# Performance work log

Measured on AMD Instinct MI355X. Metric: run time of the kernel, lower is better.

The kernel has to match this reference:

```python
import jax, jax.numpy as jnp
import numpy as np

D_MODEL = 1024
NUM_HEADS = 16
HEAD_DIM = D_MODEL // NUM_HEADS
B, S = 4, 2048


def setup_inputs() -> dict:
    key = jax.random.key(0)
    ks = jax.random.split(key, 11)
    scale = 1.0 / np.sqrt(D_MODEL)
    inp = {
        "query": jax.random.normal(ks[0], (B, S, D_MODEL), dtype=jnp.float32),
        "key": jax.random.normal(ks[1], (B, S, D_MODEL), dtype=jnp.float32),
        "value": jax.random.normal(ks[2], (B, S, D_MODEL), dtype=jnp.float32),
        "Wq": jax.random.normal(ks[3], (D_MODEL, D_MODEL), dtype=jnp.float32) * scale,
        "bq": jnp.zeros((D_MODEL,), dtype=jnp.float32),
        "Wk": jax.random.normal(ks[4], (D_MODEL, D_MODEL), dtype=jnp.float32) * scale,
        "bk": jnp.zeros((D_MODEL,), dtype=jnp.float32),
        "Wv": jax.random.normal(ks[5], (D_MODEL, D_MODEL), dtype=jnp.float32) * scale,
        "bv": jnp.zeros((D_MODEL,), dtype=jnp.float32),
        "Wo": jax.random.normal(ks[6], (D_MODEL, D_MODEL), dtype=jnp.float32) * scale,
        "bo": jnpp.zeros((D_MODEL,), dtype=jnp.float32) if False else jnp.zeros((D_MODEL,), dtype=jnp.float32),
    }
    return inp


def reference(query, key, value, Wq, bq, Wk, bk, Wv, bv, Wo, bo):
    # Linear projections (torch Linear: x @ W.T + b), split into heads: [B,H,S,Dh]
    def split_heads(x):
        b, s, _ = x.shape
        return x.reshape(b, s, NUM_HEADS, HEAD_DIM).transpose(0, 2, 1, 3)

    q = split_heads(query @ Wq.T + bq)
    k = split_heads(key @ Wk.T + bk)
    v = split_heads(value @ Wv.T + bv)

    # Explicit attention: [B,H,S,S] scores, softmax, AV
    scores = jnp.einsum("bhqd,bhkd->bhqk", q, k) / np.sqrt(HEAD_DIM).astype(np.float32)
    attn = jax.nn.softmax(scores, axis=-1)
    ctx = jnp.einsum("bhqk,bhkd->bhqd", attn, v)

    # Merge heads and output projection
    b = ctx.shape[0]
    ctx = ctx.transpose(0, 2, 1, 3).reshape(b, -1, D_MODEL)
    return ctx @ Wo.T + bo
```

## Files before the change

kernel.cpp:

```cpp
#include <hip/hip_runtime.h>
#include <stdint.h>

#define DMODEL 1024
#define NHEADS 16
#define HDIM   64
#define BB     4
#define SS     2048
#define MM     (BB*SS)
#define QKV_ELEMS ((size_t)8388608)

typedef unsigned short ushort_t;
typedef __bf16    bf16x8  __attribute__((ext_vector_type(8)));
typedef _Float16  half4   __attribute__((ext_vector_type(4)));
typedef _Float16  half2_t __attribute__((ext_vector_type(2)));
typedef float     floatx4 __attribute__((ext_vector_type(4)));

__device__ inline ushort_t f32_to_bf16(float f) {
    union { float f; uint32_t u; } v; v.f = f;
    uint32_t r = v.u + 0x7FFF + ((v.u >> 16) & 1);
    return (ushort_t)(r >> 16);
}
__device__ inline ushort_t f32_to_f16u(float f) {
    union { _Float16 h; ushort_t u; } v; v.h = (_Float16)f; return v.u;
}
__device__ inline half2_t pkrtz(float a, float b) {
    return __builtin_bit_cast(half2_t, __builtin_amdgcn_cvt_pkrtz(a, b));
}
__device__ inline void glds16(const void* g, void* l) {
    __builtin_amdgcn_global_load_lds(
        (const __attribute__((address_space(1))) unsigned int*)g,
        (__attribute__((address_space(3))) unsigned int*)l, 16, 0, 0);
}

__global__ __launch_bounds__(256) void convert_bf16(const float* __restrict__ in,
                                                    ushort_t* __restrict__ out) {
    size_t i = ((size_t)blockIdx.x * 256 + threadIdx.x) * 8;
    float4 a = *(const float4*)&in[i];
    float4 b = *(const float4*)&in[i + 4];
    ushort_t t[8];
    t[0] = f32_to_bf16(a.x); t[1] = f32_to_bf16(a.y);
    t[2] = f32_to_bf16(a.z); t[3] = f32_to_bf16(a.w);
    t[4] = f32_to_bf16(b.x); t[5] = f32_to_bf16(b.y);
    t[6] = f32_to_bf16(b.z); t[7] = f32_to_bf16(b.w);
    *(uint4*)&out[i] = *(uint4*)t;
}

__global__ __launch_bounds__(256) void convert_w3(
    const float* __restrict__ w0, const float* __restrict__ w1, const float* __restrict__ w2,
    ushort_t* __restrict__ o0, ushort_t* __restrict__ o1, ushort_t* __restrict__ o2) {
    const float* src = (blockIdx.y == 0) ? w0 : (blockIdx.y == 1) ? w1 : w2;
    ushort_t*    dst = (blockIdx.y == 0) ? o0 : (blockIdx.y == 1) ? o1 : o2;
    size_t i = ((size_t)blockIdx.x * 256 + threadIdx.x) * 8;
    float4 a = *(const float4*)&src[i];
    float4 b = *(const float4*)&src[i + 4];
    ushort_t t[8];
    t[0] = f32_to_bf16(a.x); t[1] = f32_to_bf16(a.y);
    t[2] = f32_to_bf16(a.z); t[3] = f32_to_bf16(a.w);
    t[4] = f32_to_bf16(b.x); t[5] = f32_to_bf16(b.y);
    t[6] = f32_to_bf16(b.z); t[7] = f32_to_bf16(b.w);
    *(uint4*)&dst[i] = *(uint4*)t;
}

template<int OUT>
__global__ __launch_bounds__(256) void gemm_bf16(
    const ushort_t* __restrict__ A, const ushort_t* __restrict__ W,
    const float* __restrict__ bias, void* __restrict__ O, float scale)
{
    __shared__ ushort_t As[2 * 128 * 32];
    __shared__ ushort_t Bs[2 * 128 * 32];

    const int tid  = threadIdx.x;
    const int lane = tid & 63;
    const int quad = lane >> 4;
    const int l15  = lane & 15;
    const int wid  = tid >> 6;
    const int wr   = wid >> 1, wc = wid & 1;
    const int m0   = blockIdx.y * 128;
    const int n0   = blockIdx.x * 128;

    floatx4 acc[4][4];
    #pragma unroll
    for (int i = 0; i < 4; i++)
        #pragma unroll
        for (int j = 0; j < 4; j++)
            acc[i][j] = (floatx4){0.f, 0.f, 0.f, 0.f};

    #pragma unroll
    for (int j = 0; j < 2; j++) {
        const int p = tid + j * 256, row = p >> 2, cc = p & 3;
        glds16(&A[(size_t)(m0 + row) * DMODEL + cc * 8], &As[p * 8]);
        glds16(&W[(size_t)(n0 + row) * DMODEL + cc * 8], &Bs[p * 8]);
    }

    for (int k0 = 0; k0 < DMODEL; k0 += 32) {
        const int cb = ((k0 >> 5) & 1) * (128 * 32);
        const int nbo = (128 * 32) - cb;
        __syncthreads();
        const int kn = (k0 + 32) & (DMODEL - 1);
        #pragma unroll
        for (int j = 0; j < 2; j++) {
            const int p = tid + j * 256, row = p >> 2, cc = p & 3;
            glds16(&A[(size_t)(m0 + row) * DMODEL + kn + cc * 8], &As[nbo + p * 8]);
            glds16(&W[(size_t)(n0 + row) * DMODEL + kn + cc * 8], &Bs[nbo + p * 8]);
        }
        bf16x8 af[4], bf[4];
        #pragma unroll
        for (int i = 0; i < 4; i++)
            af[i] = *(const bf16x8*)&As[cb + (wr * 64 + i * 16 + l15) * 32 + quad * 8];
        #pragma unroll
        for (int j = 0; j < 4; j++)
            bf[j] = *(const bf16x8*)&Bs[cb + (wc * 64 + j * 16 + l15) * 32 + quad * 8];
        #pragma unroll
        for (int i = 0; i < 4; i++)
            #pragma unroll
            for (int j = 0; j < 4; j++)
                acc[i][j] = __builtin_amdgcn_mfma_f32_16x16x32_bf16(af[i], bf[j], acc[i][j], 0, 0, 0);
    }

    #pragma unroll
    for (int j = 0; j < 4; j++) {
        const int n = n0 + wc * 64 + j * 16 + l15;
        const float bn = bias[n];
        #pragma unroll
        for (int i = 0; i < 4; i++) {
            #pragma unroll
            for (int r = 0; r < 4; r++) {
                const int m = m0 + wr * 64 + i * 16 + quad * 4 + r;
                float v = (acc[i][j][r] + bn) * scale;
                if (OUT == 0) {
                    const int b = m >> 11, s = m & 2047;
                    const int hh = n >> 6, dh = n & 63;
                    ((ushort_t*)O)[(((size_t)(b * NHEADS + hh)) * SS + s) * HDIM + dh] = f32_to_bf16(v);
                } else if (OUT == 1) {
                    const int b = m >> 11, s = m & 2047;
                    const int hh = n >> 6, dh = n & 63;
                    ((ushort_t*)O)[(((size_t)(b * NHEADS + hh)) * SS + s) * HDIM + dh] = f32_to_f16u(v);
                } else {
                    ((float*)O)[(size_t)m * DMODEL + n] = v;
                }
            }
        }
    }
}

__global__ __launch_bounds__(256, 4) void attn_kernel(
    const ushort_t* __restrict__ Q, const ushort_t* __restrict__ K,
    const ushort_t* __restrict__ V, ushort_t* __restrict__ ctx)
{
    constexpr int LDV = 72;
    constexpr int VOFF = 2 * 4096;
    __shared__ ushort_t smem[2 * 4096 + 2 * 64 * LDV];
    ushort_t* Tr = smem;

    const int tid  = threadIdx.x;
    const int lane = tid & 63;
    const int wid  = tid >> 6;
    const int quad = lane >> 4;
    const int l15  = lane & 15;
    const int bid  = blockIdx.x;
    const int bh   = (bid & 7) * 8 + (bid >> 7);
    const int b    = bh >> 4, h = bh & 15;
    const int q0   = ((bid >> 3) & 15) * 128 + wid * 32;

    const ushort_t* Qb = Q + (size_t)bh * SS * HDIM;
    const ushort_t* Kb = K + (size_t)bh * SS * HDIM;
    const ushort_t* Vb = V + (size_t)bh * SS * HDIM;

    bf16x8 qf[2][2];
    #pragma unroll
    for (int qt = 0; qt < 2; qt++)
        #pragma unroll
        for (int c = 0; c < 2; c++)
            qf[qt][c] = *(const bf16x8*)&Qb[(size_t)(q0 + qt * 16 + l15) * HDIM + c * 32 + quad * 8];

    floatx4 acc[2][4];
    #pragma unroll
    for (int qt = 0; qt < 2; qt++)
        #pragma unroll
        for (int dt = 0; dt < 4; dt++)
            acc[qt][dt] = (floatx4){0.f, 0.f, 0.f, 0.f};
    float mrun[2] = {-1e30f, -1e30f};
    float lrun[2] = {0.f, 0.f};

    const int kp = tid & 31;
    const int dc = tid >> 5;

    #pragma unroll
    for (int j = 0; j < 2; j++) {
        const int p = tid + j * 256, row = p >> 3, cc = (p & 7) ^ (row & 7);
        glds16(&Kb[(size_t)row * HDIM + cc * 8], &smem[p * 8]);
    }
    {
        ushort_t ua[8], ub[8];
        *(uint4*)ua = *(const uint4*)&Vb[(size_t)(2 * kp) * HDIM + dc * 8];
        *(uint4*)ub = *(const uint4*)&Vb[(size_t)(2 * kp + 1) * HDIM + dc * 8];
        #pragma unroll
        for (int i = 0; i < 8; i++)
            *(uint32_t*)&smem[VOFF + (dc * 8 + i) * LDV + 2 * kp] = (uint32_t)ua[i] | ((uint32_t)ub[i] << 16);
    }

    const half2_t one2 = {(_Float16)1.f, (_Float16)1.f};

    for (int kt = 0; kt < SS; kt += 64) {
        const int cur = ((kt >> 6) & 1);
        const int ko  = cur * 4096;
        const int kon = 4096 - ko;
        const int vo  = VOFF + cur * (64 * LDV);
        const int von = VOFF + (64 * LDV) - cur * (64 * LDV);
        __syncthreads();

        const int ktn = (kt + 64) & (SS - 1);
        #pragma unroll
        for (int j = 0; j < 2; j++) {
            const int p = tid + j * 256, row = p >> 3, cc = (p & 7) ^ (row & 7);
            glds16(&Kb[(size_t)(ktn + row) * HDIM + cc * 8], &smem[kon + p * 8]);
        }
        ushort_t ua[8], ub[8];
        *(uint4*)ua = *(const uint4*)&Vb[(size_t)(ktn + 2 * kp) * HDIM + dc * 8];
        *(uint4*)ub = *(const uint4*)&Vb[(size_t)(ktn + 2 * kp + 1) * HDIM + dc * 8];

        bf16x8 kf[4][2];
        #pragma unroll
        for (int nt = 0; nt < 4; nt++) {
            const int row = nt * 16 + l15;
            #pragma unroll
            for (int c = 0; c < 2; c++) {
                const int pos = (c * 4 + quad) ^ (row & 7);
                kf[nt][c] = *(const bf16x8*)&smem[ko + row * 64 + pos * 8];
            }
        }
        half4 vf[4][4];
        #pragma unroll
        for (int kb = 0; kb < 4; kb++)
            #pragma unroll
            for (int dt = 0; dt < 4; dt++)
                vf[kb][dt] = *(const half4*)&smem[vo + (dt * 16 + l15) * LDV + kb * 16 + quad * 4];

        #pragma unroll
        for (int qt = 0; qt < 2; qt++) {
            floatx4 s[4];
            #pragma unroll
            for (int nt = 0; nt < 4; nt++) {
                floatx4 cz = (floatx4){0.f, 0.f, 0.f, 0.f};
                cz = __builtin_amdgcn_mfma_f32_16x16x32_bf16(kf[nt][0], qf[qt][0], cz, 0, 0, 0);
                cz = __builtin_amdgcn_mfma_f32_16x16x32_bf16(kf[nt][1], qf[qt][1], cz, 0, 0, 0);
                s[nt] = cz;
            }
            float mx = s[0][0];
            #pragma unroll
            for (int nt = 0; nt < 4; nt++)
                #pragma unroll
                for (int r = 0; r < 4; r++) mx = fmaxf(mx, s[nt][r]);
            mx = fmaxf(mx, __shfl_xor(mx, 16));
            mx = fmaxf(mx, __shfl_xor(mx, 32));
            const float mnew  = fmaxf(mrun[qt], mx);
            const float alpha = __builtin_amdgcn_exp2f(mrun[qt] - mnew);
            mrun[qt] = mnew;

            float ps = 0.f;
            half4 pf[4];
            #pragma unroll
            for (int nt = 0; nt < 4; nt++) {
                const float p0 = __builtin_amdgcn_exp2f(s[nt][0] - mnew);
                const float p1 = __builtin_amdgcn_exp2f(s[nt][1] - mnew);
                const float p2 = __builtin_amdgcn_exp2f(s[nt][2] - mnew);
                const float p3 = __builtin_amdgcn_exp2f(s[nt][3] - mnew);
                const half2_t ha = pkrtz(p0, p1);
                const half2_t hb = pkrtz(p2, p3);
                ps = __builtin_amdgcn_fdot2(ha, one2, ps, false);
                ps = __builtin_amdgcn_fdot2(hb, one2, ps, false);
                union { half4 h4; half2_t h2[2]; } u;
                u.h2[0] = ha; u.h2[1] = hb;
                pf[nt] = u.h4;
            }
            ps += __shfl_xor(ps, 16);
            ps += __shfl_xor(ps, 32);
            lrun[qt] = lrun[qt] * alpha + ps;

            #pragma unroll
            for (int dt = 0; dt < 4; dt++) acc[qt][dt] *= alpha;
            #pragma unroll
            for (int kb = 0; kb < 4; kb++)
                #pragma unroll
                for (int dt = 0; dt < 4; dt++)
                    acc[qt][dt] = __builtin_amdgcn_mfma_f32_16x16x16f16(vf[kb][dt], pf[kb], acc[qt][dt], 0, 0, 0);
        }

        #pragma unroll
        for (int i = 0; i < 8; i++)
            *(uint32_t*)&smem[von + (dc * 8 + i) * LDV + 2 * kp] = (uint32_t)ua[i] | ((uint32_t)ub[i] << 16);
    }

    __syncthreads();
    const float inv0 = 1.f / lrun[0], inv1 = 1.f / lrun[1];
    ushort_t* Tw = Tr + wid * (32 * LDV);
    #pragma unroll
    for (int qt = 0; qt < 2; qt++) {
        const float inv = qt ? inv1 : inv0;
        #pragma unroll
        for (int dt = 0; dt < 4; dt++)
            #pragma unroll
            for (int r = 0; r < 4; r++)
                Tw[(qt * 16 + l15) * LDV + dt * 16 + quad * 4 + r] = f32_to_bf16(acc[qt][dt][r] * inv);
    }
    const int row = lane >> 1, hf = lane & 1;
    const ushort_t* src = Tw + row * LDV + hf * 32;
    ushort_t* dst = ctx + ((size_t)(b * SS) + q0 + row) * DMODEL + h * HDIM + hf * 32;
    #pragma unroll
    for (int i = 0; i < 4; i++)
        *(uint4*)(dst + i * 8) = *(const uint4*)(src + i * 8);
}

extern "C" void kernel_launch(void* const* d_in, const int* in_sizes, int n_in,
                              void* d_out, int out_size, void* d_ws, size_t ws_size,
                              hipStream_t stream) {
    (void)in_sizes; (void)n_in; (void)out_size; (void)ws_size;
    const float* query = (const float*)d_in[0];
    const float* key_  = (const float*)d_in[1];
    const float* value = (const float*)d_in[2];
    const float* Wq = (const float*)d_in[3];
    const float* bq = (const float*)d_in[4];
    const float* Wk = (const float*)d_in[5];
    const float* bk = (const float*)d_in[6];
    const float* Wv = (const float*)d_in[7];
    const float* bv = (const float*)d_in[8];
    const float* Wo = (const float*)d_in[9];
    const float* bo = (const float*)d_in[10];
    float* out = (float*)d_out;

    ushort_t* tmp = (ushort_t*)d_ws;
    ushort_t* Qw  = tmp + QKV_ELEMS;
    ushort_t* Kw  = Qw + QKV_ELEMS;
    ushort_t* Vw  = Kw + QKV_ELEMS;
    ushort_t* ctx = tmp;
    ushort_t* Wqb = (ushort_t*)d_out;
    ushort_t* Wkb = Wqb + 1048576;
    ushort_t* Wvb = Wkb + 1048576;
    ushort_t* Wob = Qw;

    dim3 blk(256);
    dim3 gg(DMODEL / 128, MM / 128);

    hipLaunchKernelGGL(convert_w3, dim3(512, 3), blk, 0, stream, Wq, Wk, Wv, Wqb, Wkb, Wvb);

    hipLaunchKernelGGL(convert_bf16, dim3(4096), blk, 0, stream, query, tmp);
    hipLaunchKernelGGL((gemm_bf16<0>), gg, blk, 0, stream, tmp, Wqb, bq, (void*)Qw, 0.18033688011f);
    hipLaunchKernelGGL(convert_bf16, dim3(4096), blk, 0, stream, key_, tmp);
    hipLaunchKernelGGL((gemm_bf16<0>), gg, blk, 0, stream, tmp, Wkb, bk, (void*)Kw, 1.0f);
    hipLaunchKernelGGL(convert_bf16, dim3(4096), blk, 0, stream, value, tmp);
    hipLaunchKernelGGL((gemm_bf16<1>), gg, blk, 0, stream, tmp, Wvb, bv, (void*)Vw, 1.0f);

    hipLaunchKernelGGL(attn_kernel, dim3(1024), blk, 0, stream, Qw, Kw, Vw, ctx);

    hipLaunchKernelGGL(convert_bf16, dim3(512), blk, 0, stream, Wo, Wob);
    hipLaunchKernelGGL((gemm_bf16<2>), gg, blk, 0, stream, ctx, Wob, bo, (void*)out, 1.0f);
}
```

Measured before the change: 401.6 us.

## Deepen GEMM K-step, remap block indices, and lazily rescale softmax in attention

The GEMM now stages 64-wide K slices per iteration instead of 32, which halves the number of barriers per tile at the cost of doubled shared memory. Blocks move to a 1D grid with a swizzled M/N mapping so that concurrently running blocks share weight tiles in cache. In attention, the online-softmax rescale is skipped unless some lane's new max exceeds the running max by more than 8 (log2 units), avoiding exp and accumulator multiplies on most iterations. The lazy rescale lets probabilities reach 2^8 in fp16, which risks precision loss but stays within fp16 range.

Result: slower. 529.1 us (+31.8%).

```diff
diff --git a/kernel.cpp b/kernel.cpp
--- a/kernel.cpp
+++ b/kernel.cpp
@@ -66,8 +66,8 @@
     const ushort_t* __restrict__ A, const ushort_t* __restrict__ W,
     const float* __restrict__ bias, void* __restrict__ O, float scale)
 {
-    __shared__ ushort_t As[2 * 128 * 32];
-    __shared__ ushort_t Bs[2 * 128 * 32];
+    __shared__ ushort_t As[2 * 128 * 64];
+    __shared__ ushort_t Bs[2 * 128 * 64];
 
     const int tid  = threadIdx.x;
     const int lane = tid & 63;
@@ -75,8 +75,10 @@
     const int l15  = lane & 15;
     const int wid  = tid >> 6;
     const int wr   = wid >> 1, wc = wid & 1;
-    const int m0   = blockIdx.y * 128;
-    const int n0   = blockIdx.x * 128;
+
+    const int bid  = blockIdx.x;
+    const int m0   = ((bid & 7) * 8 + ((bid >> 3) & 7)) * 128;
+    const int n0   = (bid >> 6) * 128;
 
     floatx4 acc[4][4];
     #pragma unroll
@@ -86,35 +88,42 @@
             acc[i][j] = (floatx4){0.f, 0.f, 0.f, 0.f};
 
     #pragma unroll
-    for (int j = 0; j < 2; j++) {
-        const int p = tid + j * 256, row = p >> 2, cc = p & 3;
-        glds16(&A[(size_t)(m0 + row) * DMODEL + cc * 8], &As[p * 8]);
-        glds16(&W[(size_t)(n0 + row) * DMODEL + cc * 8], &Bs[p * 8]);
-    }
-
-    for (int k0 = 0; k0 < DMODEL; k0 += 32) {
-        const int cb = ((k0 >> 5) & 1) * (128 * 32);
-        const int nbo = (128 * 32) - cb;
+    for (int r = 0; r < 4; r++) {
+        const int p = tid + (r & 1) * 256;
+        const int ks = r >> 1;
+        const int row = p >> 2, cc = p & 3;
+        glds16(&A[(size_t)(m0 + row) * DMODEL + ks * 32 + cc * 8], &As[ks * 4096 + p * 8]);
+        glds16(&W[(size_t)(n0 + row) * DMODEL + ks * 32 + cc * 8], &Bs[ks * 4096 + p * 8]);
+    }
+
+    for (int k0 = 0; k0 < DMODEL; k0 += 64) {
+        const int cb  = ((k0 >> 6) & 1) * 8192;
+        const int nbo = 8192 - cb;
         __syncthreads();
-        const int kn = (k0 + 32) & (DMODEL - 1);
-        #pragma unroll
-        for (int j = 0; j < 2; j++) {
-            const int p = tid + j * 256, row = p >> 2, cc = p & 3;
-            glds16(&A[(size_t)(m0 + row) * DMODEL + kn + cc * 8], &As[nbo + p * 8]);
-            glds16(&W[(size_t)(n0 + row) * DMODEL + kn + cc * 8], &Bs[nbo + p * 8]);
-        }
-        bf16x8 af[4], bf[4];
-        #pragma unroll
-        for (int i = 0; i < 4; i++)
-            af[i] = *(const bf16x8*)&As[cb + (wr * 64 + i * 16 + l15) * 32 + quad * 8];
-        #pragma unroll
-        for (int j = 0; j < 4; j++)
-            bf[j] = *(const bf16x8*)&Bs[cb + (wc * 64 + j * 16 + l15) * 32 + quad * 8];
-        #pragma unroll
-        for (int i = 0; i < 4; i++)
+        const int kn = (k0 + 64) & (DMODEL - 1);
+        #pragma unroll
+        for (int r = 0; r < 4; r++) {
+            const int p = tid + (r & 1) * 256;
+            const int ks = r >> 1;
+            const int row = p >> 2, cc = p & 3;
+            glds16(&A[(size_t)(m0 + row) * DMODEL + kn + ks * 32 + cc * 8], &As[nbo + ks * 4096 + p * 8]);
+            glds16(&W[(size_t)(n0 + row) * DMODEL + kn + ks * 32 + cc * 8], &Bs[nbo + ks * 4096 + p * 8]);
+        }
+        #pragma unroll
+        for (int ks = 0; ks < 2; ks++) {
+            bf16x8 af[4], bfr[4];
+            #pragma unroll
+            for (int i = 0; i < 4; i++)
+                af[i] = *(const bf16x8*)&As[cb + ks * 4096 + (wr * 64 + i * 16 + l15) * 32 + quad * 8];
             #pragma unroll
             for (int j = 0; j < 4; j++)
-                acc[i][j] = __builtin_amdgcn_mfma_f32_16x16x32_bf16(af[i], bf[j], acc[i][j], 0, 0, 0);
+                bfr[j] = *(const bf16x8*)&Bs[cb + ks * 4096 + (wc * 64 + j * 16 + l15) * 32 + quad * 8];
+            #pragma unroll
+            for (int i = 0; i < 4; i++)
+                #pragma unroll
+                for (int j = 0; j < 4; j++)
+                    acc[i][j] = __builtin_amdgcn_mfma_f32_16x16x32_bf16(af[i], bfr[j], acc[i][j], 0, 0, 0);
+        }
     }
 
     #pragma unroll
@@ -246,25 +255,33 @@
                 cz = __builtin_amdgcn_mfma_f32_16x16x32_bf16(kf[nt][1], qf[qt][1], cz, 0, 0, 0);
                 s[nt] = cz;
             }
-            float mx = s[0][0];
-            #pragma unroll
-            for (int nt = 0; nt < 4; nt++)
-                #pragma unroll
-                for (int r = 0; r < 4; r++) mx = fmaxf(mx, s[nt][r]);
+            float t0 = fmaxf(fmaxf(s[0][0], s[0][1]), fmaxf(s[0][2], s[0][3]));
+            float t1 = fmaxf(fmaxf(s[1][0], s[1][1]), fmaxf(s[1][2], s[1][3]));
+            float t2 = fmaxf(fmaxf(s[2][0], s[2][1]), fmaxf(s[2][2], s[2][3]));
+            float t3 = fmaxf(fmaxf(s[3][0], s[3][1]), fmaxf(s[3][2], s[3][3]));
+            float mx = fmaxf(fmaxf(t0, t1), fmaxf(t2, t3));
             mx = fmaxf(mx, __shfl_xor(mx, 16));
             mx = fmaxf(mx, __shfl_xor(mx, 32));
-            const float mnew  = fmaxf(mrun[qt], mx);
-            const float alpha = __builtin_amdgcn_exp2f(mrun[qt] - mnew);
-            mrun[qt] = mnew;
+
+            float mref = mrun[qt];
+            if (!__all(mx - mref <= 8.0f)) {
+                const float mnew  = fmaxf(mref, mx);
+                const float alpha = __builtin_amdgcn_exp2f(mref - mnew);
+                lrun[qt] *= alpha;
+                #pragma unroll
+                for (int dt = 0; dt < 4; dt++) acc[qt][dt] *= alpha;
+                mrun[qt] = mnew;
+                mref = mnew;
+            }
 
             float ps = 0.f;
             half4 pf[4];
             #pragma unroll
             for (int nt = 0; nt < 4; nt++) {
-                const float p0 = __builtin_amdgcn_exp2f(s[nt][0] - mnew);
-                const float p1 = __builtin_amdgcn_exp2f(s[nt][1] - mnew);
-                const float p2 = __builtin_amdgcn_exp2f(s[nt][2] - mnew);
-                const float p3 = __builtin_amdgcn_exp2f(s[nt][3] - mnew);
+                const float p0 = __builtin_amdgcn_exp2f(s[nt][0] - mref);
+                const float p1 = __builtin_amdgcn_exp2f(s[nt][1] - mref);
+                const float p2 = __builtin_amdgcn_exp2f(s[nt][2] - mref);
+                const float p3 = __builtin_amdgcn_exp2f(s[nt][3] - mref);
                 const half2_t ha = pkrtz(p0, p1);
                 const half2_t hb = pkrtz(p2, p3);
                 ps = __builtin_amdgcn_fdot2(ha, one2, ps, false);
@@ -275,10 +292,8 @@
             }
             ps += __shfl_xor(ps, 16);
             ps += __shfl_xor(ps, 32);
-            lrun[qt] = lrun[qt] * alpha + ps;
-
-            #pragma unroll
-            for (int dt = 0; dt < 4; dt++) acc[qt][dt] *= alpha;
+            lrun[qt] += ps;
+
             #pragma unroll
             for (int kb = 0; kb < 4; kb++)
                 #pragma unroll
@@ -339,7 +354,7 @@
     ushort_t* Wob = Qw;
 
     dim3 blk(256);
-    dim3 gg(DMODEL / 128, MM / 128);
+    dim3 gg(512);
 
     hipLaunchKernelGGL(convert_w3, dim3(512, 3), blk, 0, stream, Wq, Wk, Wv, Wqb, Wkb, Wvb);
 
```
